# Performance work log

Hardware: AMD Instinct MI355X
Metric: run time of the kernel (lower is better)

Reference implementation:

```python
import jax, jax.numpy as jnp
import numpy as np

BLOCK_M = 64
BLOCK_K = 64
THRES = 0.8


def setup_inputs() -> dict:
    key = jax.random.key(0)
    k1, k2 = jax.random.split(key)
    bsz, d_in, d_out = 8192, 4096, 4096
    x = jax.random.normal(k1, (bsz, d_in), dtype=jnp.float32)
    # kaiming_uniform_(a=sqrt(5)) on a (d_in, d_out) tensor -> bound = 1/sqrt(d_out)
    bound = 1.0 / np.sqrt(d_out)
    weight = jax.random.uniform(k2, (d_in, d_out), dtype=jnp.float32,
                                minval=-bound, maxval=bound)
    return {"x": x, "weight": weight}


def reference(x, weight):
    bsz, hidden = x.shape
    nm, nk = bsz // BLOCK_M, hidden // BLOCK_K
    # per-block average magnitude of activations: [nm, nk]
    blocks = jnp.abs(x).reshape(nm, BLOCK_M, nk, BLOCK_K)
    avg_mag = blocks.mean(axis=(1, 3))
    block_mask = avg_mag > THRES  # [nm, nk] bool
    # expand mask to element level and zero inactive activation blocks
    mask_elem = jnp.repeat(jnp.repeat(block_mask, BLOCK_M, axis=0), BLOCK_K, axis=1)
    x_masked = jnp.where(mask_elem, x, 0.0)
    # block-sparse masked GEMM (dense reference of the same math)
    return x_masked @ weight
```

## Files before the change

kernel.cpp:

```cpp
#include <hip/hip_runtime.h>
#include <hip/hip_bf16.h>
#include <stdint.h>

#define BSZ   8192
#define D_IN  4096
#define D_OUT 4096
#define NM    128
#define NK    64

typedef __bf16 bf16x8 __attribute__((ext_vector_type(8)));
typedef float  f32x4  __attribute__((ext_vector_type(4)));
typedef unsigned short ushort_t;

__device__ __forceinline__ ushort_t f2bf(float f) {
  union { __hip_bfloat16 h; ushort_t u; } c;
  c.h = __float2bfloat16(f);
  return c.u;
}

__device__ __forceinline__ bf16x8 ld_frag(const ushort_t* p) {
  union { uint4 u; bf16x8 b; } cv;
  cv.u = *(const uint4*)p;
  return cv.b;
}

__device__ __forceinline__ void glds16(const ushort_t* g, ushort_t* l) {
  __builtin_amdgcn_global_load_lds(
      (const __attribute__((address_space(1))) unsigned int*)g,
      (__attribute__((address_space(3))) unsigned int*)l,
      16, 0, 0);
}

__global__ __launch_bounds__(256) void mask_cast_kernel(
    const float* __restrict__ x, ushort_t* __restrict__ xb,
    int* __restrict__ mask) {
  const int kblk = blockIdx.x;
  const int mblk = blockIdx.y;
  const int tid  = threadIdx.x;
  const int lane = tid & 63;
  const int wv   = tid >> 6;
  const size_t row0 = (size_t)mblk * 64;
  const int    col0 = kblk * 64;

  float4 v[4];
  double s = 0.0;
#pragma unroll
  for (int i = 0; i < 4; ++i) {
    int j = i * 256 + tid;
    int r = j >> 4;
    int c = (j & 15) * 4;
    v[i] = *(const float4*)(x + (row0 + r) * D_IN + col0 + c);
    s += (double)fabsf(v[i].x) + (double)fabsf(v[i].y) +
         (double)fabsf(v[i].z) + (double)fabsf(v[i].w);
  }

#pragma unroll
  for (int off = 32; off > 0; off >>= 1) {
    union { double d; int i2[2]; } u;
    u.d = s;
    u.i2[0] = __shfl_xor(u.i2[0], off, 64);
    u.i2[1] = __shfl_xor(u.i2[1], off, 64);
    s += u.d;
  }

  __shared__ double wsum[4];
  __shared__ int mflag;
  if (lane == 0) wsum[wv] = s;
  __syncthreads();
  if (tid == 0) {
    double tot = wsum[0] + wsum[1] + wsum[2] + wsum[3];
    float avg = (float)(tot * (1.0 / 4096.0));
    int m = (avg > 0.8f) ? 1 : 0;
    mflag = m;
    mask[mblk * NK + kblk] = m;
  }
  __syncthreads();

  if (mflag) {
#pragma unroll
    for (int i = 0; i < 4; ++i) {
      int j = i * 256 + tid;
      int r = j >> 4;
      int c = (j & 15) * 4;
      ushort4 o = make_ushort4(f2bf(v[i].x), f2bf(v[i].y),
                               f2bf(v[i].z), f2bf(v[i].w));
      *(ushort4*)(xb + (row0 + r) * D_IN + col0 + c) = o;
    }
  }
}

__global__ __launch_bounds__(256) void wcast_transpose_kernel(
    const float* __restrict__ w, ushort_t* __restrict__ wT) {
  const int ntile = blockIdx.x;
  const int ktile = blockIdx.y;
  const int tid   = threadIdx.x;
  const int k0 = ktile * 64, n0 = ntile * 64;

  __shared__ ushort_t t[64][65];

#pragma unroll
  for (int i = 0; i < 4; ++i) {
    int j = i * 256 + tid;
    int r = j >> 4;
    int c = (j & 15) * 4;
    float4 v = *(const float4*)(w + (size_t)(k0 + r) * D_OUT + n0 + c);
    t[r][c + 0] = f2bf(v.x);
    t[r][c + 1] = f2bf(v.y);
    t[r][c + 2] = f2bf(v.z);
    t[r][c + 3] = f2bf(v.w);
  }
  __syncthreads();
#pragma unroll
  for (int i = 0; i < 4; ++i) {
    int j = i * 256 + tid;
    int r = j >> 4;
    int c = (j & 15) * 4;
    ushort4 o = make_ushort4(t[c + 0][r], t[c + 1][r], t[c + 2][r], t[c + 3][r]);
    *(ushort4*)(wT + (size_t)(n0 + r) * D_IN + k0 + c) = o;
  }
}

__global__ __launch_bounds__(256) void bsp_gemm_kernel(
    const ushort_t* __restrict__ xb, const ushort_t* __restrict__ wT,
    const int* __restrict__ mask, float* __restrict__ out) {
  const int ntile = blockIdx.x;
  const int mblk  = blockIdx.y;
  const int tid   = threadIdx.x;
  const int lane  = tid & 63;
  const int wv    = tid >> 6;
  const int m0 = mblk * 64;
  const int n0 = ntile * 256;

  __shared__ ushort_t As[64 * 64];
  __shared__ ushort_t Bs[256 * 64];
  __shared__ int nact;
  __shared__ unsigned char klist[64];

  const int* mrow = mask + mblk * NK;
  if (tid == 0) {
    int n = 0;
#pragma unroll
    for (int kb = 0; kb < NK; ++kb) {
      if (mrow[kb] != 0) klist[n++] = (unsigned char)kb;
    }
    nact = n;
  }
  __syncthreads();
  const int na = nact;

  f32x4 acc[4][4] = {};

  const int lr  = lane >> 3;
  const int lcs = ((lane & 7) ^ (lane >> 3)) * 8;
  const int q   = lane >> 4;
  const int l15 = lane & 15;
  const int sx  = l15 & 7;

  for (int ki = 0; ki < na; ++ki) {
    const int kb = klist[ki];
    const int k0 = kb * 64;

#pragma unroll
    for (int t = 0; t < 2; ++t) {
      int rb = wv * 16 + t * 8;
      glds16(xb + (size_t)(m0 + rb + lr) * D_IN + k0 + lcs, &As[rb * 64]);
    }
#pragma unroll
    for (int t = 0; t < 8; ++t) {
      int rb = wv * 64 + t * 8;
      glds16(wT + (size_t)(n0 + rb + lr) * D_IN + k0 + lcs, &Bs[rb * 64]);
    }
    __syncthreads();

#pragma unroll
    for (int c = 0; c < 2; ++c) {
      const int sw = ((c * 4 + q) ^ sx) * 8;
      bf16x8 a[4], b[4];
#pragma unroll
      for (int i = 0; i < 4; ++i)
        a[i] = ld_frag(&As[(i * 16 + l15) * 64 + sw]);
#pragma unroll
      for (int j = 0; j < 4; ++j)
        b[j] = ld_frag(&Bs[(wv * 64 + j * 16 + l15) * 64 + sw]);
#pragma unroll
      for (int i = 0; i < 4; ++i)
#pragma unroll
        for (int j = 0; j < 4; ++j)
          acc[i][j] = __builtin_amdgcn_mfma_f32_16x16x32_bf16(
              a[i], b[j], acc[i][j], 0, 0, 0);
    }
    __syncthreads();
  }

#pragma unroll
  for (int i = 0; i < 4; ++i) {
#pragma unroll
    for (int j = 0; j < 4; ++j) {
#pragma unroll
      for (int r = 0; r < 4; ++r) {
        int row = m0 + i * 16 + q * 4 + r;
        int col = n0 + wv * 64 + j * 16 + l15;
        out[(size_t)row * D_OUT + col] = acc[i][j][r];
      }
    }
  }
}

extern "C" void kernel_launch(void* const* d_in, const int* in_sizes, int n_in,
                              void* d_out, int out_size, void* d_ws, size_t ws_size,
                              hipStream_t stream) {
  const float* x = (const float*)d_in[0];
  const float* w = (const float*)d_in[1];

  ushort_t* xb  = (ushort_t*)d_ws;
  ushort_t* wT  = (ushort_t*)((char*)d_ws + (size_t)BSZ * D_IN * 2);
  int*      msk = (int*)((char*)d_ws + (size_t)BSZ * D_IN * 2 + (size_t)D_IN * D_OUT * 2);
  float*    out = (float*)d_out;

  hipLaunchKernelGGL(mask_cast_kernel, dim3(NK, NM), dim3(256), 0, stream,
                     x, xb, msk);
  hipLaunchKernelGGL(wcast_transpose_kernel, dim3(64, 64), dim3(256), 0, stream,
                     w, wT);
  hipLaunchKernelGGL(bsp_gemm_kernel, dim3(D_OUT / 256, NM), dim3(256), 0, stream,
                     xb, wT, msk, out);
}
```

Measured before the change: 440.3 us.

## Merge prep kernels and widen GEMM N-tile to 512 with swapped grid order

Merges the activation mask/cast kernel and the weight cast/transpose kernel into one launch, dispatching on block index and sharing LDS through a union. The GEMM tile grows from 64x256 to 64x512, giving 128 accumulators per thread, and the grid is reordered so M-blocks vary fastest, which improves reuse of the weight tile across consecutive blocks. B fragments are now loaded one at a time inside the MFMA loop to reduce register pressure, and launch bounds request 2 blocks per CU. The larger tile doubles LDS use to about 72KB and raises VGPR pressure, and cuts the GEMM grid to 1024 blocks, which may hurt occupancy and load balance.

```diff
diff --git a/kernel.cpp b/kernel.cpp
--- a/kernel.cpp
+++ b/kernel.cpp
@@ -31,108 +31,112 @@
       16, 0, 0);
 }
 
-__global__ __launch_bounds__(256) void mask_cast_kernel(
-    const float* __restrict__ x, ushort_t* __restrict__ xb,
+__global__ __launch_bounds__(256) void prep_kernel(
+    const float* __restrict__ x, const float* __restrict__ w,
+    ushort_t* __restrict__ xb, ushort_t* __restrict__ wT,
     int* __restrict__ mask) {
-  const int kblk = blockIdx.x;
-  const int mblk = blockIdx.y;
-  const int tid  = threadIdx.x;
-  const int lane = tid & 63;
-  const int wv   = tid >> 6;
-  const size_t row0 = (size_t)mblk * 64;
-  const int    col0 = kblk * 64;
-
-  float4 v[4];
-  double s = 0.0;
-#pragma unroll
-  for (int i = 0; i < 4; ++i) {
-    int j = i * 256 + tid;
-    int r = j >> 4;
-    int c = (j & 15) * 4;
-    v[i] = *(const float4*)(x + (row0 + r) * D_IN + col0 + c);
-    s += (double)fabsf(v[i].x) + (double)fabsf(v[i].y) +
-         (double)fabsf(v[i].z) + (double)fabsf(v[i].w);
-  }
-
-#pragma unroll
-  for (int off = 32; off > 0; off >>= 1) {
-    union { double d; int i2[2]; } u;
-    u.d = s;
-    u.i2[0] = __shfl_xor(u.i2[0], off, 64);
-    u.i2[1] = __shfl_xor(u.i2[1], off, 64);
-    s += u.d;
-  }
-
-  __shared__ double wsum[4];
-  __shared__ int mflag;
-  if (lane == 0) wsum[wv] = s;
-  __syncthreads();
-  if (tid == 0) {
-    double tot = wsum[0] + wsum[1] + wsum[2] + wsum[3];
-    float avg = (float)(tot * (1.0 / 4096.0));
-    int m = (avg > 0.8f) ? 1 : 0;
-    mflag = m;
-    mask[mblk * NK + kblk] = m;
-  }
-  __syncthreads();
-
-  if (mflag) {
+  __shared__ union {
+    struct { double wsum[4]; int mflag; } m;
+    ushort_t t[64][65];
+  } sm;
+
+  const int bid = blockIdx.x;
+  const int tid = threadIdx.x;
+
+  if (bid < NM * NK) {
+    const int kblk = bid & (NK - 1);
+    const int mblk = bid >> 6;
+    const int lane = tid & 63;
+    const int wv   = tid >> 6;
+    const size_t row0 = (size_t)mblk * 64;
+    const int    col0 = kblk * 64;
+
+    float4 v[4];
+    double s = 0.0;
 #pragma unroll
     for (int i = 0; i < 4; ++i) {
       int j = i * 256 + tid;
       int r = j >> 4;
       int c = (j & 15) * 4;
-      ushort4 o = make_ushort4(f2bf(v[i].x), f2bf(v[i].y),
-                               f2bf(v[i].z), f2bf(v[i].w));
-      *(ushort4*)(xb + (row0 + r) * D_IN + col0 + c) = o;
-    }
-  }
-}
-
-__global__ __launch_bounds__(256) void wcast_transpose_kernel(
-    const float* __restrict__ w, ushort_t* __restrict__ wT) {
-  const int ntile = blockIdx.x;
-  const int ktile = blockIdx.y;
-  const int tid   = threadIdx.x;
-  const int k0 = ktile * 64, n0 = ntile * 64;
-
-  __shared__ ushort_t t[64][65];
-
-#pragma unroll
-  for (int i = 0; i < 4; ++i) {
-    int j = i * 256 + tid;
-    int r = j >> 4;
-    int c = (j & 15) * 4;
-    float4 v = *(const float4*)(w + (size_t)(k0 + r) * D_OUT + n0 + c);
-    t[r][c + 0] = f2bf(v.x);
-    t[r][c + 1] = f2bf(v.y);
-    t[r][c + 2] = f2bf(v.z);
-    t[r][c + 3] = f2bf(v.w);
-  }
-  __syncthreads();
-#pragma unroll
-  for (int i = 0; i < 4; ++i) {
-    int j = i * 256 + tid;
-    int r = j >> 4;
-    int c = (j & 15) * 4;
-    ushort4 o = make_ushort4(t[c + 0][r], t[c + 1][r], t[c + 2][r], t[c + 3][r]);
-    *(ushort4*)(wT + (size_t)(n0 + r) * D_IN + k0 + c) = o;
-  }
-}
-
-__global__ __launch_bounds__(256) void bsp_gemm_kernel(
+      v[i] = *(const float4*)(x + (row0 + r) * D_IN + col0 + c);
+      s += (double)fabsf(v[i].x) + (double)fabsf(v[i].y) +
+           (double)fabsf(v[i].z) + (double)fabsf(v[i].w);
+    }
+
+#pragma unroll
+    for (int off = 32; off > 0; off >>= 1) {
+      union { double d; int i2[2]; } u;
+      u.d = s;
+      u.i2[0] = __shfl_xor(u.i2[0], off, 64);
+      u.i2[1] = __shfl_xor(u.i2[1], off, 64);
+      s += u.d;
+    }
+
+    if (lane == 0) sm.m.wsum[wv] = s;
+    __syncthreads();
+    if (tid == 0) {
+      double tot = sm.m.wsum[0] + sm.m.wsum[1] + sm.m.wsum[2] + sm.m.wsum[3];
+      float avg = (float)(tot * (1.0 / 4096.0));
+      int m = (avg > 0.8f) ? 1 : 0;
+      sm.m.mflag = m;
+      mask[mblk * NK + kblk] = m;
+    }
+    __syncthreads();
+
+    if (sm.m.mflag) {
+#pragma unroll
+      for (int i = 0; i < 4; ++i) {
+        int j = i * 256 + tid;
+        int r = j >> 4;
+        int c = (j & 15) * 4;
+        ushort4 o = make_ushort4(f2bf(v[i].x), f2bf(v[i].y),
+                                 f2bf(v[i].z), f2bf(v[i].w));
+        *(ushort4*)(xb + (row0 + r) * D_IN + col0 + c) = o;
+      }
+    }
+  } else {
+    const int tt = bid - NM * NK;
+    const int ntile = tt & 63;
+    const int ktile = tt >> 6;
+    const int k0 = ktile * 64, n0 = ntile * 64;
+
+#pragma unroll
+    for (int i = 0; i < 4; ++i) {
+      int j = i * 256 + tid;
+      int r = j >> 4;
+      int c = (j & 15) * 4;
+      float4 v = *(const float4*)(w + (size_t)(k0 + r) * D_OUT + n0 + c);
+      sm.t[r][c + 0] = f2bf(v.x);
+      sm.t[r][c + 1] = f2bf(v.y);
+      sm.t[r][c + 2] = f2bf(v.z);
+      sm.t[r][c + 3] = f2bf(v.w);
+    }
+    __syncthreads();
+#pragma unroll
+    for (int i = 0; i < 4; ++i) {
+      int j = i * 256 + tid;
+      int r = j >> 4;
+      int c = (j & 15) * 4;
+      ushort4 o = make_ushort4(sm.t[c + 0][r], sm.t[c + 1][r],
+                               sm.t[c + 2][r], sm.t[c + 3][r]);
+      *(ushort4*)(wT + (size_t)(n0 + r) * D_IN + k0 + c) = o;
+    }
+  }
+}
+
+__global__ __launch_bounds__(256, 2) void bsp_gemm_kernel(
     const ushort_t* __restrict__ xb, const ushort_t* __restrict__ wT,
     const int* __restrict__ mask, float* __restrict__ out) {
-  const int ntile = blockIdx.x;
-  const int mblk  = blockIdx.y;
+  const int mblk  = blockIdx.x;
+  const int ntile = blockIdx.y;
   const int tid   = threadIdx.x;
   const int lane  = tid & 63;
   const int wv    = tid >> 6;
   const int m0 = mblk * 64;
-  const int n0 = ntile * 256;
+  const int n0 = ntile * 512;
 
   __shared__ ushort_t As[64 * 64];
-  __shared__ ushort_t Bs[256 * 64];
+  __shared__ ushort_t Bs[512 * 64];
   __shared__ int nact;
   __shared__ unsigned char klist[64];
 
@@ -148,7 +152,7 @@
   __syncthreads();
   const int na = nact;
 
-  f32x4 acc[4][4] = {};
+  f32x4 acc[4][8] = {};
 
   const int lr  = lane >> 3;
   const int lcs = ((lane & 7) ^ (lane >> 3)) * 8;
@@ -166,8 +170,8 @@
       glds16(xb + (size_t)(m0 + rb + lr) * D_IN + k0 + lcs, &As[rb * 64]);
     }
 #pragma unroll
-    for (int t = 0; t < 8; ++t) {
-      int rb = wv * 64 + t * 8;
+    for (int t = 0; t < 16; ++t) {
+      int rb = wv * 128 + t * 8;
       glds16(wT + (size_t)(n0 + rb + lr) * D_IN + k0 + lcs, &Bs[rb * 64]);
     }
     __syncthreads();
@@ -175,19 +179,18 @@
 #pragma unroll
     for (int c = 0; c < 2; ++c) {
       const int sw = ((c * 4 + q) ^ sx) * 8;
-      bf16x8 a[4], b[4];
+      bf16x8 a[4];
 #pragma unroll
       for (int i = 0; i < 4; ++i)
         a[i] = ld_frag(&As[(i * 16 + l15) * 64 + sw]);
 #pragma unroll
-      for (int j = 0; j < 4; ++j)
-        b[j] = ld_frag(&Bs[(wv * 64 + j * 16 + l15) * 64 + sw]);
-#pragma unroll
-      for (int i = 0; i < 4; ++i)
-#pragma unroll
-        for (int j = 0; j < 4; ++j)
+      for (int j = 0; j < 8; ++j) {
+        bf16x8 b = ld_frag(&Bs[(wv * 128 + j * 16 + l15) * 64 + sw]);
+#pragma unroll
+        for (int i = 0; i < 4; ++i)
           acc[i][j] = __builtin_amdgcn_mfma_f32_16x16x32_bf16(
-              a[i], b[j], acc[i][j], 0, 0, 0);
+              a[i], b, acc[i][j], 0, 0, 0);
+      }
     }
     __syncthreads();
   }
@@ -195,11 +198,11 @@
 #pragma unroll
   for (int i = 0; i < 4; ++i) {
 #pragma unroll
-    for (int j = 0; j < 4; ++j) {
+    for (int j = 0; j < 8; ++j) {
 #pragma unroll
       for (int r = 0; r < 4; ++r) {
         int row = m0 + i * 16 + q * 4 + r;
-        int col = n0 + wv * 64 + j * 16 + l15;
+        int col = n0 + wv * 128 + j * 16 + l15;
         out[(size_t)row * D_OUT + col] = acc[i][j][r];
       }
     }
@@ -217,10 +220,8 @@
   int*      msk = (int*)((char*)d_ws + (size_t)BSZ * D_IN * 2 + (size_t)D_IN * D_OUT * 2);
   float*    out = (float*)d_out;
 
-  hipLaunchKernelGGL(mask_cast_kernel, dim3(NK, NM), dim3(256), 0, stream,
-                     x, xb, msk);
-  hipLaunchKernelGGL(wcast_transpose_kernel, dim3(64, 64), dim3(256), 0, stream,
-                     w, wT);
-  hipLaunchKernelGGL(bsp_gemm_kernel, dim3(D_OUT / 256, NM), dim3(256), 0, stream,
+  hipLaunchKernelGGL(prep_kernel, dim3(NM * NK + 64 * 64), dim3(256), 0, stream,
+                     x, w, xb, wT, msk);
+  hipLaunchKernelGGL(bsp_gemm_kernel, dim3(NM, D_OUT / 512), dim3(256), 0, stream,
                      xb, wT, msk, out);
 }
```

After: 441.6 us. About the same (+0.3%).
